# Kernel tuning notes

Measured on AMD Instinct MI355X. Metric: run time of the kernel, lower is better.

Reference implementation:

```python
import jax, jax.numpy as jnp
import numpy as np

B, C, T = 4, 80, 800            # batch, n_mels (= d_model), frames
DEPTH, D_IN, N, DT_R, K = 12, 160, 16, 5, 4  # layers, expand*d_model, d_state, dt_rank, conv kernel
ATT, EMB, EPS = 128, 192, 1e-12

LP_NAMES = ['ln1_g','ln1_b','in_proj','conv_w','conv_b','x_proj','dt_w','dt_b','A_log','D','out_proj','ln2_g','ln2_b','ff_w1','ff_b1','ff_w2','ff_b2']
PP_NAMES = ['att_w1','att_b1','bn1_g','bn1_b','bn1_m','bn1_v','att_w2','att_b2','bn2_g','bn2_b','bn2_m','bn2_v','fc_w','fc_b']


def _layernorm(x, g, b, eps=1e-5):
    mu = x.mean(-1, keepdims=True)
    v = ((x - mu) ** 2).mean(-1, keepdims=True)
    return (x - mu) * jax.lax.rsqrt(v + eps) * g + b


def _mamba(x, p):
    # x: [B, L, d_model] -> standard Mamba selective-scan block
    xz = x @ p['in_proj']                              # [B,L,2*D_IN]
    xc, z = jnp.split(xz, 2, axis=-1)
    xp = jnp.pad(xc, ((0, 0), (K - 1, 0), (0, 0)))     # causal left pad
    xc = jax.lax.conv_general_dilated(
        xp, p['conv_w'], (1,), 'VALID',
        dimension_numbers=('NWC', 'WIO', 'NWC'),
        feature_group_count=D_IN) + p['conv_b']
    xc = jax.nn.silu(xc)
    dbc = xc @ p['x_proj']                             # [B,L,DT_R+2N]
    dt, Bm, Cm = jnp.split(dbc, [DT_R, DT_R + N], axis=-1)
    dt = jax.nn.softplus(dt @ p['dt_w'] + p['dt_b'])   # [B,L,D_IN]
    A = -jnp.exp(p['A_log'])                           # [D_IN,N]

    def step(h, inp):
        x_t, dt_t, B_t, C_t = inp                      # [B,D],[B,D],[B,N],[B,N]
        dA = jnp.exp(dt_t[..., None] * A)              # [B,D,N]
        h = dA * h + (dt_t * x_t)[..., None] * B_t[:, None, :]
        y = jnp.einsum('bdn,bn->bd', h, C_t)
        return h, y

    h0 = jnp.zeros((x.shape[0], D_IN, N), x.dtype)
    xs = tuple(jnp.swapaxes(a, 0, 1) for a in (xc, dt, Bm, Cm))
    _, ys = jax.lax.scan(step, h0, xs)
    y = jnp.swapaxes(ys, 0, 1) + xc * p['D']
    y = y * jax.nn.silu(z)
    return y @ p['out_proj']


def _encoder(x, p):
    xn = _layernorm(x, p['ln1_g'], p['ln1_b'])
    fwd = _mamba(xn, p)
    bwd = jnp.flip(_mamba(jnp.flip(xn, 1), p), 1)      # bidirectional, shared weights
    m = _layernorm(fwd + bwd, p['ln2_g'], p['ln2_b'])
    ff = jax.nn.gelu(m @ p['ff_w1'] + p['ff_b1'], approximate=False) @ p['ff_w2'] + p['ff_b2']
    return ff + x


def _forward(feat, lp, pp):
    feat = feat - feat.mean(-1, keepdims=True)         # CMN
    x = jnp.swapaxes(feat, 1, 2)                       # [B,T,C]

    def body(xc, p):
        return _encoder(xc, p), None

    x, _ = jax.lax.scan(body, x, lp)                   # 12 stacked layers
    x = jnp.swapaxes(x, 1, 2)                          # [B,C,T]

    # Attentive statistics pooling (global context)
    mean = x.mean(-1, keepdims=True)
    std = jnp.sqrt(jnp.maximum(((x - mean) ** 2).mean(-1, keepdims=True), EPS))
    g = jnp.concatenate([x, jnp.broadcast_to(mean, x.shape), jnp.broadcast_to(std, x.shape)], axis=1)  # [B,3C,T]
    a = jnp.einsum('bct,cd->bdt', g, pp['att_w1']) + pp['att_b1'][:, None]
    a = jax.nn.relu(a)
    a = (a - pp['bn1_m'][:, None]) * jax.lax.rsqrt(pp['bn1_v'][:, None] + 1e-5) * pp['bn1_g'][:, None] + pp['bn1_b'][:, None]
    a = jnp.tanh(a)
    a = jnp.einsum('bdt,dc->bct', a, pp['att_w2']) + pp['att_b2'][:, None]
    w = jax.nn.softmax(a, axis=-1)
    mu = jnp.sum(w * x, axis=-1)
    sg = jnp.sqrt(jnp.maximum(jnp.sum(w * x * x, axis=-1) - mu ** 2, EPS))
    pooled = jnp.concatenate([mu, sg], axis=-1)        # [B,2C]

    pooled = (pooled - pp['bn2_m']) * jax.lax.rsqrt(pp['bn2_v'] + 1e-5) * pp['bn2_g'] + pp['bn2_b']
    return pooled @ pp['fc_w'] + pp['fc_b']            # [B,EMB] source embedding


def setup_inputs() -> dict:
    key = jax.random.key(0)
    ks = jax.random.split(key, 12)

    def w(k, shape, s=0.05):
        return jax.random.normal(k, shape, jnp.float32) * s

    L = DEPTH
    return {
        'feat': jax.random.normal(ks[0], (B, C, T), jnp.float32),
        'ln1_g': jnp.ones((L, C)), 'ln1_b': jnp.zeros((L, C)),
        'in_proj': w(ks[1], (L, C, 2 * D_IN)),
        'conv_w': w(ks[2], (L, K, 1, D_IN), 0.2),
        'conv_b': jnp.zeros((L, D_IN)),
        'x_proj': w(ks[3], (L, D_IN, DT_R + 2 * N)),
        'dt_w': w(ks[4], (L, DT_R, D_IN), 0.2),
        'dt_b': jnp.full((L, D_IN), -2.0),
        'A_log': jnp.tile(jnp.log(jnp.arange(1, N + 1, dtype=jnp.float32)), (L, D_IN, 1)),
        'D': jnp.ones((L, D_IN)),
        'out_proj': w(ks[5], (L, D_IN, C)),
        'ln2_g': jnp.ones((L, C)), 'ln2_b': jnp.zeros((L, C)),
        'ff_w1': w(ks[6], (L, C, 4 * C)), 'ff_b1': jnp.zeros((L, 4 * C)),
        'ff_w2': w(ks[7], (L, 4 * C, C)), 'ff_b2': jnp.zeros((L, C)),
        'att_w1': w(ks[8], (3 * C, ATT)), 'att_b1': jnp.zeros((ATT,)),
        'bn1_g': jnp.ones((ATT,)), 'bn1_b': jnp.zeros((ATT,)),
        'bn1_m': jnp.zeros((ATT,)), 'bn1_v': jnp.ones((ATT,)),
        'att_w2': w(ks[9], (ATT, C)), 'att_b2': jnp.zeros((C,)),
        'bn2_g': jnp.ones((2 * C,)), 'bn2_b': jnp.zeros((2 * C,)),
        'bn2_m': jnp.zeros((2 * C,)), 'bn2_v': jnp.ones((2 * C,)),
        'fc_w': w(ks[10], (2 * C, EMB)), 'fc_b': jnp.zeros((EMB,)),
        'aug': 0,
    }


def reference(feat, ln1_g, ln1_b, in_proj, conv_w, conv_b, x_proj, dt_w, dt_b, A_log, D, out_proj, ln2_g, ln2_b, ff_w1, ff_b1, ff_w2, ff_b2, att_w1, att_b1, bn1_g, bn1_b, bn1_m, bn1_v, att_w2, att_b2, bn2_g, bn2_b, bn2_m, bn2_v, fc_w, fc_b, aug):
    lp = dict(zip(LP_NAMES, (ln1_g, ln1_b, in_proj, conv_w, conv_b, x_proj, dt_w, dt_b, A_log, D, out_proj, ln2_g, ln2_b, ff_w1, ff_b1, ff_w2, ff_b2)))
    pp = dict(zip(PP_NAMES, (att_w1, att_b1, bn1_g, bn1_b, bn1_m, bn1_v, att_w2, att_b2, bn2_g, bn2_b, bn2_m, bn2_v, fc_w, fc_b)))
    # aug == 0 -> SpecAug skipped (eval path); speaker branch (frozen, no_grad) omitted
    return _forward(feat, lp, pp)
```

## Files before the change

kernel.cpp:

```cpp
#include <hip/hip_runtime.h>
#include <hip/hip_bf16.h>

#define B_ 4
#define C_ 80
#define T_ 800
#define R_ 3200
#define DIN 160
#define NST 16
#define NC 16
#define LCH 50

typedef const float* fp;

__device__ __forceinline__ void g2l16(const float* g, float* l) {
  __builtin_amdgcn_global_load_lds(
      (const __attribute__((address_space(1))) void*)g,
      (__attribute__((address_space(3))) void*)l,
      16, 0, 0);
}

__device__ __forceinline__ float blockSum(float v, float* sb) {
  for (int o = 32; o; o >>= 1) v += __shfl_xor(v, o);
  __syncthreads();
  if ((threadIdx.x & 63) == 0) sb[threadIdx.x >> 6] = v;
  __syncthreads();
  return sb[0] + sb[1] + sb[2] + sb[3];
}
__device__ __forceinline__ float blockMax(float v, float* sb) {
  for (int o = 32; o; o >>= 1) v = fmaxf(v, __shfl_xor(v, o));
  __syncthreads();
  if ((threadIdx.x & 63) == 0) sb[threadIdx.x >> 6] = v;
  __syncthreads();
  return fmaxf(fmaxf(sb[0], sb[1]), fmaxf(sb[2], sb[3]));
}

__global__ __launch_bounds__(256) void prepw_k(fp in_proj, fp ff_w1,
    fp ln1_g, fp ln1_b, fp ln2_g, fp ln2_b, fp ff_b1,
    float* __restrict__ wp, float* __restrict__ uvb) {
  int idx = blockIdx.x * 256 + threadIdx.x;
  int c = idx % 320, lm = idx / 320;
  int mat = lm & 1, l = lm >> 1;
  fp W = (mat ? ff_w1 : in_proj) + l * 25600;
  fp g = (mat ? ln2_g : ln1_g) + l * 80;
  fp b = (mat ? ln2_b : ln1_b) + l * 80;
  float* wpo = wp + lm * 25600;
  float u = 0.f, v = 0.f;
  for (int k = 0; k < 80; ++k) {
    float w = W[k * 320 + c];
    float gw = g[k] * w;
    wpo[k * 320 + c] = gw;
    u += gw;
    v += b[k] * w;
  }
  if (mat) v += ff_b1[l * 320 + c];
  uvb[lm * 640 + c] = u;
  uvb[lm * 640 + 320 + c] = v;
}

__global__ __launch_bounds__(256) void prepx_k(fp x_proj, float* __restrict__ xpt) {
  int idx = blockIdx.x * 256 + threadIdx.x;
  if (idx >= 71040) return;
  int l = idx / 5920, r = idx % 5920;
  int c = r / 160, k = r % 160;
  xpt[idx] = x_proj[l * 5920 + k * 37 + c];
}

__global__ __launch_bounds__(256) void prept_k(fp out_proj, fp ff_w2,
    float* __restrict__ wot, float* __restrict__ w2t) {
  int idx = blockIdx.x * 256 + threadIdx.x;
  if (idx < 153600) {
    int l = idx / 12800, r = idx % 12800;
    int c = r / 160, k = r % 160;
    wot[idx] = out_proj[l * 12800 + k * 80 + c];
  } else if (idx < 153600 + 307200) {
    int j = idx - 153600;
    int l = j / 25600, r = j % 25600;
    int c = r / 320, k = r % 320;
    w2t[j] = ff_w2[l * 25600 + k * 80 + c];
  }
}

__global__ __launch_bounds__(256) void cmn_k(fp feat, float* __restrict__ x) {
  int bc = blockIdx.x;
  int b = bc / C_, c = bc % C_;
  const float* f = feat + (b * C_ + c) * T_;
  __shared__ float sb[4];
  int tid = threadIdx.x;
  float v[4]; float s = 0.f;
  #pragma unroll
  for (int i = 0; i < 4; ++i) {
    int t = tid + i * 256;
    v[i] = (t < T_) ? f[t] : 0.f;
    s += v[i];
  }
  s = blockSum(s, sb);
  float mu = s * (1.f / T_);
  #pragma unroll
  for (int i = 0; i < 4; ++i) {
    int t = tid + i * 256;
    if (t < T_) x[(b * T_ + t) * C_ + c] = v[i] - mu;
  }
}

__global__ __launch_bounds__(256) void rstat_k(const float* __restrict__ in,
                                               float* __restrict__ must) {
  int row = blockIdx.x * 16 + (threadIdx.x >> 4);
  int c16 = threadIdx.x & 15;
  float s = 0.f, q = 0.f;
  #pragma unroll
  for (int m = 0; m < 5; ++m) {
    float v = in[row * 80 + c16 + 16 * m];
    s += v; q += v * v;
  }
  s += __shfl_xor(s, 1); s += __shfl_xor(s, 2);
  s += __shfl_xor(s, 4); s += __shfl_xor(s, 8);
  q += __shfl_xor(q, 1); q += __shfl_xor(q, 2);
  q += __shfl_xor(q, 4); q += __shfl_xor(q, 8);
  if (c16 == 0) {
    float mu = s * 0.0125f;
    float rs = rsqrtf(fmaxf(q * 0.0125f - mu * mu, 0.f) + 1e-5f);
    must[row * 2] = mu;
    must[row * 2 + 1] = rs;
  }
}

template<int EPI>
__global__ __launch_bounds__(256, 4) void gw_k(const float* __restrict__ A,
    fp W, fp uv, const float* __restrict__ must, const float* __restrict__ extra,
    float* __restrict__ out, int N) {
  __shared__ float SL[5120 + 4 * 1280];
  int tid = threadIdx.x, wv = tid >> 6, ln = tid & 63;
  int bid = blockIdx.x;
// ... 16 lines not shown
  __syncthreads();
  int rq = ln >> 4, c16 = ln & 15;
  float acc[4][4] = {};
  #pragma unroll 2
  for (int k4 = 0; k4 < 80; k4 += 4) {
    float4 a[4], w[4];
    #pragma unroll
    for (int i = 0; i < 4; ++i)
      a[i] = *(const float4*)&As[(rq * 4 + i) * 80 + k4];
    #pragma unroll
    for (int kk = 0; kk < 4; ++kk)
      w[kk] = *(const float4*)&SL[(k4 + kk) * 64 + c16 * 4];
    #pragma unroll
    for (int i = 0; i < 4; ++i) {
      acc[i][0] += a[i].x*w[0].x + a[i].y*w[1].x + a[i].z*w[2].x + a[i].w*w[3].x;
      acc[i][1] += a[i].x*w[0].y + a[i].y*w[1].y + a[i].z*w[2].y + a[i].w*w[3].y;
      acc[i][2] += a[i].x*w[0].z + a[i].y*w[1].z + a[i].z*w[2].z + a[i].w*w[3].z;
      acc[i][3] += a[i].x*w[0].w + a[i].y*w[1].w + a[i].z*w[2].w + a[i].w*w[3].w;
    }
  }
  float ua[4], va[4];
  if (EPI != 3) {
    *(float4*)ua = *(const float4*)&uv[c0 + c16 * 4];
    *(float4*)va = *(const float4*)&uv[N + c0 + c16 * 4];
  }
  #pragma unroll
  for (int i = 0; i < 4; ++i) {
    int row = row0 + rq * 4 + i;
    float mu = 0.f, rs = 1.f;
    if (EPI != 3) {
      float2 ms = *(const float2*)&must[row * 2];
      mu = ms.x; rs = ms.y;
    }
    float4 o;
    float* op = &o.x;
    #pragma unroll
    for (int j = 0; j < 4; ++j) {
      float v = acc[i][j];
      if (EPI == 3) {
        int c = c0 + c16 * 4 + j;
        v += extra[(row / T_) * 128 + c];
        v = fmaxf(v, 0.f);
        v = v * extra[512 + c] + extra[640 + c];
        v = tanhf(v);
      } else {
        v = rs * v - mu * rs * ua[j] + va[j];
      }
      op[j] = v;
    }
    *(float4*)&out[row * N + c0 + c16 * 4] = o;
  }
}

template<int EPI, int KCH, int NKC, int SUM2, int STAT>
__global__ __launch_bounds__(256, 4) void gc_k(const float* __restrict__ A,
    fp W, fp bias, const float* __restrict__ extra, float* __restrict__ out,
    int Astride, float* __restrict__ must) {
  constexpr int P = KCH + 4;
  __shared__ float As[16 * P];
  __shared__ float Wt[80 * P];
  int tid = threadIdx.x;
  int row0 = blockIdx.x * 16;
  int rr = tid >> 4, c16 = tid & 15;
  float acc[5] = {};
  for (int kc = 0; kc < NKC; ++kc) {
    if (kc) __syncthreads();
    #pragma unroll
    for (int i = 0; i < 16 * KCH / 256; ++i) {
      int e = tid + i * 256;
      int r = e / KCH, k = e - r * KCH;
      float v;
      if (SUM2) v = A[(row0 + r) * 320 + k] + A[(row0 + r) * 320 + 160 + k];
      else      v = A[(row0 + r) * Astride + kc * KCH + k];
      As[r * P + k] = v;
    }
    #pragma unroll
    for (int i = 0; i < KCH * 80 / 256; ++i) {
      int e = tid + i * 256;
      int kr = e / 80, c = e - kr * 80;
      Wt[c * P + kr] = W[(kc * KCH + kr) * 80 + c];
    }
    __syncthreads();
    #pragma unroll 4
    for (int k4 = 0; k4 < KCH; k4 += 4) {
      float4 a = *(const float4*)&As[rr * P + k4];
      #pragma unroll
      for (int m = 0; m < 5; ++m) {
        float4 w = *(const float4*)&Wt[(c16 + 16 * m) * P + k4];
        acc[m] += a.x * w.x + a.y * w.y + a.z * w.z + a.w * w.w;
      }
    }
  }
  int row = row0 + rr;
  #pragma unroll
  for (int m = 0; m < 5; ++m) {
    int c = c16 + 16 * m;
    float v = acc[m];
    if (EPI == 2) v += bias[c] + extra[row * 80 + c];
    else if (EPI == 4) v += bias[c];
    out[row * 80 + c] = v;
  }
}

__global__ __launch_bounds__(256, 2) void gof_k(const float* __restrict__ yg,
    fp wotl, fp w1pl, fp uv1, float* __restrict__ g1) {
  __shared__ float As[16 * 164];
  __shared__ float Wt[80 * 164];
  __shared__ float sl[16 * 84];
  __shared__ float ss[32];
  int tid = threadIdx.x, row0 = blockIdx.x * 16, rr = tid >> 4, c16 = tid & 15;
  #pragma unroll
  for (int i = 0; i < 10; ++i) {
    int e = tid + i * 256; int r = e / 160, k = e - r * 160;
    As[r * 164 + k] = yg[(row0 + r) * 320 + k] + yg[(row0 + r) * 320 + 160 + k];
  }
  #pragma unroll
  for (int i = 0; i < 50; ++i) {
    int e = tid + i * 256; int c = e / 160, k = e - c * 160;
    Wt[c * 164 + k] = wotl[e];
  }
  __syncthreads();
  float acc[5] = {};
  #pragma unroll 4
  for (int k4 = 0; k4 < 160; k4 += 4) {
    float4 a = *(const float4*)&As[rr * 164 + k4];
    #pragma unroll
    for (int m = 0; m < 5; ++m) {
      float4 w = *(const float4*)&Wt[(c16 + 16 * m) * 164 + k4];
      acc[m] += a.x * w.x + a.y * w.y + a.z * w.z + a.w * w.w;
    }
  }
  float s = 0.f, q = 0.f;
  #pragma unroll
  for (int m = 0; m < 5; ++m) {
    float v = acc[m];
    sl[rr * 84 + c16 + 16 * m] = v;
    s += v; q += v * v;
  }
  s += __shfl_xor(s, 1); s += __shfl_xor(s, 2);
  s += __shfl_xor(s, 4); s += __shfl_xor(s, 8);
  q += __shfl_xor(q, 1); q += __shfl_xor(q, 2);
  q += __shfl_xor(q, 4); q += __shfl_xor(q, 8);
  if (c16 == 0) {
    float mu = s * 0.0125f;
    ss[rr * 2] = mu;
    ss[rr * 2 + 1] = rsqrtf(fmaxf(q * 0.0125f - mu * mu, 0.f) + 1e-5f);
  }
  for (int h = 0; h < 2; ++h) {
    __syncthreads();
    #pragma unroll
    for (int i = 0; i < 50; ++i) {
      int e = tid + i * 256; int kr = e / 160, c = e - kr * 160;
      Wt[kr * 164 + c] = w1pl[kr * 320 + h * 160 + c];
    }
    __syncthreads();
    float mu = ss[rr * 2], rs = ss[rr * 2 + 1];
    float a2[10] = {};
    for (int k = 0; k < 80; k += 4) {
      float4 av = *(const float4*)&sl[rr * 84 + k];
      #pragma unroll
      for (int m = 0; m < 10; ++m) {
        int c = c16 + 16 * m;
        a2[m] += av.x * Wt[k * 164 + c] + av.y * Wt[(k + 1) * 164 + c]
               + av.z * Wt[(k + 2) * 164 + c] + av.w * Wt[(k + 3) * 164 + c];
      }
    }
    #pragma unroll
    for (int m = 0; m < 10; ++m) {
      int c = h * 160 + c16 + 16 * m;
      float v = rs * a2[m] - mu * rs * uv1[c] + uv1[320 + c];
      v = 0.5f * v * (1.f + erff(v * 0.70710678118f));
      g1[(row0 + rr) * 320 + c] = v;
    }
  }
}

template<int LAST>
__global__ __launch_bounds__(256, 2) void gfi_k(const float* __restrict__ g1,
    fp w2tl, fp fb2, float* __restrict__ x, fp wpn, fp uvn,
    float* __restrict__ xz) {
  __shared__ float As[16 * 164];
  __shared__ float Wt[80 * 164];
  __shared__ float xn[16 * 84];
  __shared__ float ss[32];
  int tid = threadIdx.x, row0 = blockIdx.x * 16, rr = tid >> 4, c16 = tid & 15;
  float acc[5] = {};
  for (int kc = 0; kc < 2; ++kc) {
    if (kc) __syncthreads();
    #pragma unroll
    for (int i = 0; i < 10; ++i) {
      int e = tid + i * 256; int r = e / 160, k = e - r * 160;
      As[r * 164 + k] = g1[(row0 + r) * 320 + kc * 160 + k];
    }
    #pragma unroll
    for (int i = 0; i < 50; ++i) {
      int e = tid + i * 256; int c = e / 160, k = e - c * 160;
      Wt[c * 164 + k] = w2tl[c * 320 + kc * 160 + k];
    }
    __syncthreads();
    #pragma unroll 4
    for (int k4 = 0; k4 < 160; k4 += 4) {
      float4 a = *(const float4*)&As[rr * 164 + k4];
      #pragma unroll
      for (int m = 0; m < 5; ++m) {
        float4 w = *(const float4*)&Wt[(c16 + 16 * m) * 164 + k4];
        acc[m] += a.x * w.x + a.y * w.y + a.z * w.z + a.w * w.w;
      }
    }
  }
  float s = 0.f, q = 0.f;
  #pragma unroll
  for (int m = 0; m < 5; ++m) {
    int c = c16 + 16 * m;
    float v = acc[m] + fb2[c] + x[(row0 + rr) * 80 + c];
    x[(row0 + rr) * 80 + c] = v;
    xn[rr * 84 + c] = v;
    s += v; q += v * v;
  }
  if (!LAST) {
    s += __shfl_xor(s, 1); s += __shfl_xor(s, 2);
    s += __shfl_xor(s, 4); s += __shfl_xor(s, 8);
    q += __shfl_xor(q, 1); q += __shfl_xor(q, 2);
    q += __shfl_xor(q, 4); q += __shfl_xor(q, 8);
    if (c16 == 0) {
      float mu = s * 0.0125f;
      ss[rr * 2] = mu;
      ss[rr * 2 + 1] = rsqrtf(fmaxf(q * 0.0125f - mu * mu, 0.f) + 1e-5f);
    }
    for (int h = 0; h < 2; ++h) {
      __syncthreads();
      #pragma unroll
      for (int i = 0; i < 50; ++i) {
        int e = tid + i * 256; int kr = e / 160, c = e - kr * 160;
        Wt[kr * 164 + c] = wpn[kr * 320 + h * 160 + c];
      }
      __syncthreads();
      float mu = ss[rr * 2], rs = ss[rr * 2 + 1];
      float a2[10] = {};
      for (int k = 0; k < 80; k += 4) {
        float4 av = *(const float4*)&xn[rr * 84 + k];
        #pragma unroll
        for (int m = 0; m < 10; ++m) {
          int c = c16 + 16 * m;
          a2[m] += av.x * Wt[k * 164 + c] + av.y * Wt[(k + 1) * 164 + c]
                 + av.z * Wt[(k + 2) * 164 + c] + av.w * Wt[(k + 3) * 164 + c];
        }
      }
      #pragma unroll
      for (int m = 0; m < 10; ++m) {
        int c = h * 160 + c16 + 16 * m;
        xz[(row0 + rr) * 320 + c] = rs * a2[m] - mu * rs * uvn[c] + uvn[320 + c];
      }
    }
  }
}

__global__ __launch_bounds__(256) void cxf_k(const float* __restrict__ xz,
    fp cw, fp cb, fp xptl, fp dtw, fp dtb,
    float* __restrict__ xcf, float* __restrict__ xcbb,
    float* __restrict__ dbc2, float* __restrict__ dt2) {
  __shared__ float As[16 * 164];
  __shared__ float xpT[37 * 164];
  __shared__ float dbcl[16 * 40];
  int bi = blockIdx.x;
  int tc = bi % 50; int rem = bi / 50;
  int b = rem & 3, dir = rem >> 2;
  int t0 = tc * 16;
  int tid = threadIdx.x;
  #pragma unroll
  for (int i = 0; i < 24; ++i) {
    int e = tid + i * 256;
    if (e < 5920) {
      int c = e / 160, k = e - c * 160;
      xpT[c * 164 + k] = xptl[e];
    }
  }
  float* xco = dir ? xcbb : xcf;
  #pragma unroll
  for (int i = 0; i < 3; ++i) {
    int e = tid + i * 256;
    if (e < 640) {
      int ii = e / 40, d4 = (e - ii * 40) * 4;
      int t = t0 + ii;
      float4 acc = *(const float4*)&cb[d4];
      #pragma unroll
      for (int k = 0; k < 4; ++k) {
        int tt = t - 3 + k;
        if (tt >= 0) {
          int src = dir ? (T_ - 1 - tt) : tt;
          float4 xv = *(const float4*)&xz[(b * T_ + src) * 320 + d4];
          float4 wv = *(const float4*)&cw[k * DIN + d4];
          acc.x += wv.x * xv.x; acc.y += wv.y * xv.y;
          acc.z += wv.z * xv.z; acc.w += wv.w * xv.w;
        }
      }
      float4 o;
      o.x = acc.x / (1.f + __expf(-acc.x));
      o.y = acc.y / (1.f + __expf(-acc.y));
      o.z = acc.z / (1.f + __expf(-acc.z));
      o.w = acc.w / (1.f + __expf(-acc.w));
      *(float4*)&As[ii * 164 + d4] = o;
      *(float4*)&xco[(b * T_ + t) * DIN + d4] = o;
    }
  }
  __syncthreads();
  int rr = tid >> 4, c16 = tid & 15;
  int grow0 = dir * R_ + b * T_ + t0;
  {
    float a0 = 0.f, a1 = 0.f, a2 = 0.f;
    for (int k4 = 0; k4 < 160; k4 += 4) {
      float4 a = *(const float4*)&As[rr * 164 + k4];
      float4 w0 = *(const float4*)&xpT[c16 * 164 + k4];
      float4 w1 = *(const float4*)&xpT[(c16 + 16) * 164 + k4];
      a0 += a.x * w0.x + a.y * w0.y + a.z * w0.z + a.w * w0.w;
      a1 += a.x * w1.x + a.y * w1.y + a.z * w1.z + a.w * w1.w;
      if (c16 < 5) {
        float4 w2 = *(const float4*)&xpT[(c16 + 32) * 164 + k4];
        a2 += a.x * w2.x + a.y * w2.y + a.z * w2.z + a.w * w2.w;
      }
    }
    dbcl[rr * 40 + c16] = a0;
    dbcl[rr * 40 + c16 + 16] = a1;
    dbc2[(grow0 + rr) * 37 + c16] = a0;
    dbc2[(grow0 + rr) * 37 + c16 + 16] = a1;
    if (c16 < 5) {
      dbcl[rr * 40 + c16 + 32] = a2;
      dbc2[(grow0 + rr) * 37 + c16 + 32] = a2;
    }
  }
  __syncthreads();
  #pragma unroll
  for (int i = 0; i < 10; ++i) {
    int e = tid + i * 256;
    int ii = e / 160, d = e - ii * 160;
    float v = dtb[d];
    #pragma unroll
    for (int m = 0; m < 5; ++m) v += dbcl[ii * 40 + m] * dtw[m * DIN + d];
    v = fmaxf(v, 0.f) + __logf(1.f + __expf(-fabsf(v)));
    dt2[(grow0 + ii) * DIN + d] = v;
  }
}

__global__ __launch_bounds__(256) void scanA_k(const float* __restrict__ dt2,
    const float* __restrict__ xcf, const float* __restrict__ xcbb,
    const float* __restrict__ dbc2, fp A_log,
    float* __restrict__ hend, float* __restrict__ pprod) {
  int bi = blockIdx.x;
  int cch = bi % NC; int rem = bi / NC;
  int dblk = rem % 10; rem /= 10;
  int b = rem % 4; int dir = rem / 4;
  int d0 = dblk * 16;
  int tid = threadIdx.x, dl = tid >> 4, n = tid & 15;
  int d = d0 + dl;
  float Areg = -__expf(A_log[d * NST + n]);
  __shared__ float sdt[LCH][16], sdx[LCH][16], sB[LCH][16];
  const float* xc = dir ? xcbb : xcf;
  int rbase = dir * R_ + b * T_ + cch * LCH;
  int rloc0 = b * T_ + cch * LCH;
  for (int e = tid; e < LCH * 16; e += 256) {
    int i = e >> 4, jj = e & 15;
    int grow = rbase + i;
    float dtv = dt2[grow * DIN + d0 + jj];
    sdt[i][jj] = dtv;
    sdx[i][jj] = dtv * xc[(rloc0 + i) * DIN + d0 + jj];
    sB[i][jj]  = dbc2[grow * 37 + 5 + jj];
  }
  __syncthreads();
  float h = 0.f, dts = 0.f;
  #pragma unroll 2
  for (int i = 0; i < LCH; ++i) {
    float dtv = sdt[i][dl];
    float a = __expf(dtv * Areg);
    h = a * h + sdx[i][dl] * sB[i][n];
    dts += dtv;
  }
  hend[bi * 256 + tid] = h;
  pprod[bi * 256 + tid] = __expf(dts * Areg);
}

__global__ __launch_bounds__(256) void scanC_k(const float* __restrict__ dt2,
    const float* __restrict__ dbc2, const float* __restrict__ xcf,
    const float* __restrict__ xcbb, const float* __restrict__ xz,
    fp A_log, fp Dp, const float* __restrict__ hend,
    const float* __restrict__ pprod, float* __restrict__ ygcat) {
  int bi = blockIdx.x;
  int cch = bi % NC; int rem = bi / NC;
  int dblk = rem % 10; rem /= 10;
  int b = rem % 4; int dir = rem / 4;
  int d0 = dblk * 16;
  int tid = threadIdx.x, dl = tid >> 4, n = tid & 15;
  int d = d0 + dl;
  float Areg = -__expf(A_log[d * NST + n]);
  __shared__ float sdt[LCH][16], sdx[LCH][16], sB[LCH][16], sC[LCH][16];
  __shared__ float sY[LCH][16];
  const float* xc = dir ? xcbb : xcf;
  int rbase = dir * R_ + b * T_ + cch * LCH;
  int rloc0 = b * T_ + cch * LCH;
  int sbase = (bi / NC) * (NC * 256) + tid;
  float h = 0.f;
  #pragma unroll
  for (int cc = 0; cc < NC; ++cc) {
    float p = pprod[sbase + cc * 256];
    float e = hend[sbase + cc * 256];
    if (cc < cch) h = p * h + e;
  }
  for (int e = tid; e < LCH * 16; e += 256) {
    int i = e >> 4, jj = e & 15;
    int grow = rbase + i;
    float dtv = dt2[grow * DIN + d0 + jj];
    sdt[i][jj] = dtv;
    sdx[i][jj] = dtv * xc[(rloc0 + i) * DIN + d0 + jj];
    sB[i][jj]  = dbc2[grow * 37 + 5 + jj];
    sC[i][jj]  = dbc2[grow * 37 + 21 + jj];
  }
  __syncthreads();
  for (int i = 0; i < LCH; ++i) {
    float a = __expf(sdt[i][dl] * Areg);
    h = a * h + sdx[i][dl] * sB[i][n];
    float y = h * sC[i][n];
    y += __shfl_xor(y, 1);
    y += __shfl_xor(y, 2);
    y += __shfl_xor(y, 4);
    y += __shfl_xor(y, 8);
    if (n == 0) sY[i][dl] = y;
  }
  __syncthreads();
  for (int e = tid; e < LCH * 16; e += 256) {
    int i = e >> 4, jj = e & 15;
    int t = cch * LCH + i;
    int rloc = b * T_ + t;
    float xcv = xc[rloc * DIN + d0 + jj];
    int orow = dir ? (b * T_ + (T_ - 1 - t)) : rloc;
    float z = xz[orow * 320 + 160 + d0 + jj];
    float sg = 1.f / (1.f + __expf(-z));
    ygcat[orow * 320 + dir * 160 + d0 + jj] = (sY[i][jj] + xcv * Dp[d0 + jj]) * (z * sg);
  }
}

__global__ __launch_bounds__(256) void stats_k(const float* __restrict__ x,
                                               float* __restrict__ meanv, float* __restrict__ stdv) {
  int bc = blockIdx.x; int b = bc / C_, c = bc % C_;
  __shared__ float sb[4];
  int tid = threadIdx.x;
  float v[4]; float s = 0.f;
  #pragma unroll
  for (int i = 0; i < 4; ++i) {
    int t = tid + i * 256;
    v[i] = (t < T_) ? x[(b * T_ + t) * C_ + c] : 0.f;
    s += v[i];
  }
  s = blockSum(s, sb);
  float mu = s * (1.f / T_);
  float q = 0.f;
  #pragma unroll
  for (int i = 0; i < 4; ++i) {
    int t = tid + i * 256;
    if (t < T_) { float dd = v[i] - mu; q += dd * dd; }
  }
  q = blockSum(q, sb);
  if (tid == 0) { meanv[bc] = mu; stdv[bc] = sqrtf(fmaxf(q * (1.f / T_), 1e-12f)); }
}

__global__ __launch_bounds__(256) void prep_k(const float* __restrict__ meanv,
    const float* __restrict__ stdv, fp w1, fp ab1, fp g1p, fp b1p, fp m1p, fp v1p,
    float* __restrict__ pack) {
  int idx = blockIdx.x * 256 + threadIdx.x;
  if (idx < 512) {
    int b = idx / 128, dcol = idx % 128;
    float acc = ab1[dcol];
    for (int c = 0; c < C_; ++c) {
      acc += meanv[b * C_ + c] * w1[(C_ + c) * 128 + dcol];
      acc += stdv[b * C_ + c] * w1[(2 * C_ + c) * 128 + dcol];
    }
    pack[idx] = acc;
  } else if (idx < 640) {
    int dcol = idx - 512;
    float kv = g1p[dcol] * rsqrtf(v1p[dcol] + 1e-5f);
    pack[512 + dcol] = kv;
    pack[640 + dcol] = b1p[dcol] - m1p[dcol] * kv;
  }
}

__global__ __launch_bounds__(256) void pool_k(const float* __restrict__ x,
    const float* __restrict__ scores, fp g2, fp b2, fp m2, fp v2,
    float* __restrict__ pooledn) {
  int bc = blockIdx.x; int b = bc / C_, c = bc % C_;
  __shared__ float sb[4];
  int tid = threadIdx.x;
// ... 24 lines not shown
    pooledn[b * 160 + j1] = (sg - m2[j1]) * rsqrtf(v2[j1] + 1e-5f) * g2[j1] + b2[j1];
  }
}

__global__ __launch_bounds__(256) void fc_k(const float* __restrict__ pooledn, fp fw, fp fb,
                                            float* __restrict__ out) {
  int idx = blockIdx.x * 256 + threadIdx.x;
  if (idx >= 4 * 192) return;
  int b = idx / 192, e = idx % 192;
  float acc = fb[e];
  for (int i = 0; i < 160; ++i) acc += pooledn[b * 160 + i] * fw[i * 192 + e];
  out[idx] = acc;
}

extern "C" void kernel_launch(void* const* d_in, const int* in_sizes, int n_in,
                              void* d_out, int out_size, void* d_ws, size_t ws_size,
                              hipStream_t stream) {
  fp feat   = (fp)d_in[0];
  fp ln1_g  = (fp)d_in[1];  fp ln1_b  = (fp)d_in[2];
  fp in_proj= (fp)d_in[3];
  fp conv_w = (fp)d_in[4];  fp conv_b = (fp)d_in[5];
  fp x_proj = (fp)d_in[6];
  fp dt_w   = (fp)d_in[7];  fp dt_b   = (fp)d_in[8];
  fp A_log  = (fp)d_in[9];  fp Dp     = (fp)d_in[10];
  fp out_proj=(fp)d_in[11];
  fp ln2_g  = (fp)d_in[12]; fp ln2_b  = (fp)d_in[13];
  fp ff_w1  = (fp)d_in[14]; fp ff_b1  = (fp)d_in[15];
  fp ff_w2  = (fp)d_in[16]; fp ff_b2  = (fp)d_in[17];
  fp att_w1 = (fp)d_in[18]; fp att_b1 = (fp)d_in[19];
  fp bn1_g  = (fp)d_in[20]; fp bn1_b  = (fp)d_in[21];
  fp bn1_m  = (fp)d_in[22]; fp bn1_v  = (fp)d_in[23];
  fp att_w2 = (fp)d_in[24]; fp att_b2 = (fp)d_in[25];
  fp bn2_g  = (fp)d_in[26]; fp bn2_b  = (fp)d_in[27];
  fp bn2_m  = (fp)d_in[28]; fp bn2_v  = (fp)d_in[29];
  fp fc_w   = (fp)d_in[30]; fp fc_b   = (fp)d_in[31];

  float* ws   = (float*)d_ws;
  float* x    = ws;
  float* xz   = ws + 256000;
  float* xcf  = ws + 1280000;
  float* xcb  = ws + 1792000;
  float* dbc2 = ws + 2304000;
  float* dt2  = ws + 2540800;
  float* hend = ws + 3564800;
  float* pprod= ws + 3892480;
  float* ygcat= ws + 4220160;
  float* meanv= ws + 5244160;
  float* stdv = ws + 5244480;
  float* pack = ws + 5244800;
  float* pooledn = ws + 5245568;
  float* wp   = ws + 5246208;
  float* uvb  = ws + 5860608;
  float* mst_x= ws + 5875968;
  float* xpt  = ws + 5882368;
  float* wot  = ws + 5953408;
  float* w2t  = ws + 6107008;
  float* g1   = xz;
  float* a1b  = hend;
  float* sc   = dt2;

  prepw_k<<<30, 256, 0, stream>>>(in_proj, ff_w1, ln1_g, ln1_b, ln2_g, ln2_b,
                                  ff_b1, wp, uvb);
  prepx_k<<<278, 256, 0, stream>>>(x_proj, xpt);
  prept_k<<<1800, 256, 0, stream>>>(out_proj, ff_w2, wot, w2t);
  cmn_k<<<320, 256, 0, stream>>>(feat, x);
  rstat_k<<<200, 256, 0, stream>>>(x, mst_x);
  gw_k<0><<<250, 256, 0, stream>>>(x, wp, uvb, mst_x, nullptr, xz, 320);

  for (int l = 0; l < 12; ++l) {
    cxf_k<<<400, 256, 0, stream>>>(xz, conv_w + l * 640, conv_b + l * 160,
                                   xpt + l * 5920, dt_w + l * 800, dt_b + l * 160,
                                   xcf, xcb, dbc2, dt2);
    scanA_k<<<1280, 256, 0, stream>>>(dt2, xcf, xcb, dbc2, A_log + l * 2560, hend, pprod);
    scanC_k<<<1280, 256, 0, stream>>>(dt2, dbc2, xcf, xcb, xz, A_log + l * 2560,
                                      Dp + l * 160, hend, pprod, ygcat);
    gof_k<<<200, 256, 0, stream>>>(ygcat, wot + l * 12800, wp + (2 * l + 1) * 25600,
                                   uvb + (2 * l + 1) * 640, g1);
    if (l < 11)
      gfi_k<0><<<200, 256, 0, stream>>>(g1, w2t + l * 25600, ff_b2 + l * 80, x,
                                        wp + (2 * l + 2) * 25600,
                                        uvb + (2 * l + 2) * 640, xz);
    else
      gfi_k<1><<<200, 256, 0, stream>>>(g1, w2t + l * 25600, ff_b2 + l * 80, x,
                                        wp, uvb, xz);
  }

  stats_k<<<320, 256, 0, stream>>>(x, meanv, stdv);
  prep_k<<<3, 256, 0, stream>>>(meanv, stdv, att_w1, att_b1, bn1_g, bn1_b, bn1_m, bn1_v, pack);
  gw_k<3><<<100, 256, 0, stream>>>(x, att_w1, nullptr, nullptr, pack, a1b, 128);
  gc_k<4, 128, 1, 0, 0><<<200, 256, 0, stream>>>(a1b, att_w2, att_b2, nullptr, sc, 128, nullptr);
  pool_k<<<320, 256, 0, stream>>>(x, sc, bn2_g, bn2_b, bn2_m, bn2_v, pooledn);
  fc_k<<<3, 256, 0, stream>>>(pooledn, fc_w, fc_b, (float*)d_out);
}
```

Baseline: 1.262 ms.

## Pre-pad weight tiles and stage them via direct global-to-LDS loads

A prep kernel now writes every per-layer weight matrix (out_proj, ff_w1 halves, ff_w2 halves, next-layer in_proj halves, x_proj) into the exact padded shared-memory layout, with stride 164. The GEMM kernels can then copy them straight into LDS with 16-byte global_load_lds instead of per-element transposing loads. The scan kernels likewise stage dt, x, B and C with 4-byte global_load_lds, and the scanC epilogue reuses the staged x instead of reloading it. The aim is to cut VGPR round trips and address math during staging. The cost is extra prep work and a larger workspace for the padded weight copies.

```diff
diff --git a/kernel.cpp b/kernel.cpp
--- a/kernel.cpp
+++ b/kernel.cpp
@@ -17,6 +17,26 @@
       (const __attribute__((address_space(1))) void*)g,
       (__attribute__((address_space(3))) void*)l,
       16, 0, 0);
+}
+__device__ __forceinline__ void g2l4(const float* g, float* l) {
+  __builtin_amdgcn_global_load_lds(
+      (const __attribute__((address_space(1))) void*)g,
+      (__attribute__((address_space(3))) void*)l,
+      4, 0, 0);
+}
+
+template<int NF4>
+__device__ __forceinline__ void stageN(float* dst, const float* src, int tid) {
+  int wv = tid >> 6, ln = tid & 63;
+  constexpr int NP = (NF4 + 255) / 256;
+  #pragma unroll
+  for (int i = 0; i < NP; ++i) {
+    int cbase = i * 256 + wv * 64;
+    if (cbase + ln < NF4) {
+      int lo = __builtin_amdgcn_readfirstlane(cbase * 4);
+      g2l16(src + (cbase + ln) * 4, dst + lo);
+    }
+  }
 }
 
 __device__ __forceinline__ float blockSum(float v, float* sb) {
@@ -57,27 +77,38 @@
   uvb[lm * 640 + 320 + c] = v;
 }
 
-__global__ __launch_bounds__(256) void prepx_k(fp x_proj, float* __restrict__ xpt) {
+__global__ __launch_bounds__(256) void prepg_k(fp out_proj, fp ff_w2,
+    const float* __restrict__ wp, float* __restrict__ wotp,
+    float* __restrict__ w1pp, float* __restrict__ w2tp, float* __restrict__ wpnp) {
   int idx = blockIdx.x * 256 + threadIdx.x;
-  if (idx >= 71040) return;
-  int l = idx / 5920, r = idx % 5920;
-  int c = r / 160, k = r % 160;
-  xpt[idx] = x_proj[l * 5920 + k * 37 + c];
-}
-
-__global__ __launch_bounds__(256) void prept_k(fp out_proj, fp ff_w2,
-    float* __restrict__ wot, float* __restrict__ w2t) {
+  if (idx >= 1102080) return;
+  int l = idx / 91840, r = idx % 91840;
+  if (r < 13120) {
+    int c = r / 164, k = r % 164;
+    wotp[l * 13120 + r] = (k < 160) ? out_proj[l * 12800 + k * 80 + c] : 0.f;
+  } else if (r < 39360) {
+    int r2 = r - 13120; int h = r2 / 13120, r3 = r2 % 13120;
+    int kr = r3 / 164, cq = r3 % 164;
+    w1pp[l * 26240 + r2] = (cq < 160) ? wp[(2 * l + 1) * 25600 + kr * 320 + h * 160 + cq] : 0.f;
+  } else if (r < 65600) {
+    int r2 = r - 39360; int h = r2 / 13120, r3 = r2 % 13120;
+    int c = r3 / 164, k = r3 % 164;
+    w2tp[l * 26240 + r2] = (k < 160) ? ff_w2[l * 25600 + (h * 160 + k) * 80 + c] : 0.f;
+  } else {
+    int r2 = r - 65600; int h = r2 / 13120, r3 = r2 % 13120;
+    int kr = r3 / 164, cq = r3 % 164;
+    float v = 0.f;
+    if (l < 11 && cq < 160) v = wp[(2 * l + 2) * 25600 + kr * 320 + h * 160 + cq];
+    wpnp[l * 26240 + r2] = v;
+  }
+}
+
+__global__ __launch_bounds__(256) void prepx_k(fp x_proj, float* __restrict__ xptp) {
   int idx = blockIdx.x * 256 + threadIdx.x;
-  if (idx < 153600) {
-    int l = idx / 12800, r = idx % 12800;
-    int c = r / 160, k = r % 160;
-    wot[idx] = out_proj[l * 12800 + k * 80 + c];
-  } else if (idx < 153600 + 307200) {
-    int j = idx - 153600;
-    int l = j / 25600, r = j % 25600;
-    int c = r / 320, k = r % 320;
-    w2t[j] = ff_w2[l * 25600 + k * 80 + c];
-  }
+  if (idx >= 72816) return;
+  int l = idx / 6068, r = idx % 6068;
+  int c = r / 164, k = r % 164;
+  xptp[idx] = (k < 160) ? x_proj[l * 5920 + k * 37 + c] : 0.f;
 }
 
 __global__ __launch_bounds__(256) void cmn_k(fp feat, float* __restrict__ x) {
@@ -200,10 +231,9 @@
   }
 }
 
-template<int EPI, int KCH, int NKC, int SUM2, int STAT>
+template<int EPI, int KCH, int NKC>
 __global__ __launch_bounds__(256, 4) void gc_k(const float* __restrict__ A,
-    fp W, fp bias, const float* __restrict__ extra, float* __restrict__ out,
-    int Astride, float* __restrict__ must) {
+    fp W, fp bias, float* __restrict__ out, int Astride) {
   constexpr int P = KCH + 4;
   __shared__ float As[16 * P];
   __shared__ float Wt[80 * P];
@@ -217,10 +247,7 @@
     for (int i = 0; i < 16 * KCH / 256; ++i) {
       int e = tid + i * 256;
       int r = e / KCH, k = e - r * KCH;
-      float v;
-      if (SUM2) v = A[(row0 + r) * 320 + k] + A[(row0 + r) * 320 + 160 + k];
-      else      v = A[(row0 + r) * Astride + kc * KCH + k];
-      As[r * P + k] = v;
+      As[r * P + k] = A[(row0 + r) * Astride + kc * KCH + k];
     }
     #pragma unroll
     for (int i = 0; i < KCH * 80 / 256; ++i) {
@@ -244,162 +271,8 @@
   for (int m = 0; m < 5; ++m) {
     int c = c16 + 16 * m;
     float v = acc[m];
-    if (EPI == 2) v += bias[c] + extra[row * 80 + c];
-    else if (EPI == 4) v += bias[c];
+    if (EPI == 4) v += bias[c];
     out[row * 80 + c] = v;
-  }
-}
-
-__global__ __launch_bounds__(256, 2) void gof_k(const float* __restrict__ yg,
-    fp wotl, fp w1pl, fp uv1, float* __restrict__ g1) {
-  __shared__ float As[16 * 164];
-  __shared__ float Wt[80 * 164];
-  __shared__ float sl[16 * 84];
-  __shared__ float ss[32];
-  int tid = threadIdx.x, row0 = blockIdx.x * 16, rr = tid >> 4, c16 = tid & 15;
-  #pragma unroll
-  for (int i = 0; i < 10; ++i) {
-    int e = tid + i * 256; int r = e / 160, k = e - r * 160;
-    As[r * 164 + k] = yg[(row0 + r) * 320 + k] + yg[(row0 + r) * 320 + 160 + k];
-  }
-  #pragma unroll
-  for (int i = 0; i < 50; ++i) {
-    int e = tid + i * 256; int c = e / 160, k = e - c * 160;
-    Wt[c * 164 + k] = wotl[e];
-  }
-  __syncthreads();
-  float acc[5] = {};
-  #pragma unroll 4
-  for (int k4 = 0; k4 < 160; k4 += 4) {
-    float4 a = *(const float4*)&As[rr * 164 + k4];
-    #pragma unroll
-    for (int m = 0; m < 5; ++m) {
-      float4 w = *(const float4*)&Wt[(c16 + 16 * m) * 164 + k4];
-      acc[m] += a.x * w.x + a.y * w.y + a.z * w.z + a.w * w.w;
-    }
-  }
-  float s = 0.f, q = 0.f;
-  #pragma unroll
-  for (int m = 0; m < 5; ++m) {
-    float v = acc[m];
-    sl[rr * 84 + c16 + 16 * m] = v;
-    s += v; q += v * v;
-  }
-  s += __shfl_xor(s, 1); s += __shfl_xor(s, 2);
-  s += __shfl_xor(s, 4); s += __shfl_xor(s, 8);
-  q += __shfl_xor(q, 1); q += __shfl_xor(q, 2);
-  q += __shfl_xor(q, 4); q += __shfl_xor(q, 8);
-  if (c16 == 0) {
-    float mu = s * 0.0125f;
-    ss[rr * 2] = mu;
-    ss[rr * 2 + 1] = rsqrtf(fmaxf(q * 0.0125f - mu * mu, 0.f) + 1e-5f);
-  }
-  for (int h = 0; h < 2; ++h) {
-    __syncthreads();
-    #pragma unroll
-    for (int i = 0; i < 50; ++i) {
-      int e = tid + i * 256; int kr = e / 160, c = e - kr * 160;
-      Wt[kr * 164 + c] = w1pl[kr * 320 + h * 160 + c];
-    }
-    __syncthreads();
-    float mu = ss[rr * 2], rs = ss[rr * 2 + 1];
-    float a2[10] = {};
-    for (int k = 0; k < 80; k += 4) {
-      float4 av = *(const float4*)&sl[rr * 84 + k];
-      #pragma unroll
-      for (int m = 0; m < 10; ++m) {
-        int c = c16 + 16 * m;
-        a2[m] += av.x * Wt[k * 164 + c] + av.y * Wt[(k + 1) * 164 + c]
-               + av.z * Wt[(k + 2) * 164 + c] + av.w * Wt[(k + 3) * 164 + c];
-      }
-    }
-    #pragma unroll
-    for (int m = 0; m < 10; ++m) {
-      int c = h * 160 + c16 + 16 * m;
-      float v = rs * a2[m] - mu * rs * uv1[c] + uv1[320 + c];
-      v = 0.5f * v * (1.f + erff(v * 0.70710678118f));
-      g1[(row0 + rr) * 320 + c] = v;
-    }
-  }
-}
-
-template<int LAST>
-__global__ __launch_bounds__(256, 2) void gfi_k(const float* __restrict__ g1,
-    fp w2tl, fp fb2, float* __restrict__ x, fp wpn, fp uvn,
-    float* __restrict__ xz) {
-  __shared__ float As[16 * 164];
-  __shared__ float Wt[80 * 164];
-  __shared__ float xn[16 * 84];
-  __shared__ float ss[32];
-  int tid = threadIdx.x, row0 = blockIdx.x * 16, rr = tid >> 4, c16 = tid & 15;
-  float acc[5] = {};
-  for (int kc = 0; kc < 2; ++kc) {
-    if (kc) __syncthreads();
-    #pragma unroll
-    for (int i = 0; i < 10; ++i) {
-      int e = tid + i * 256; int r = e / 160, k = e - r * 160;
-      As[r * 164 + k] = g1[(row0 + r) * 320 + kc * 160 + k];
-    }
-    #pragma unroll
-    for (int i = 0; i < 50; ++i) {
-      int e = tid + i * 256; int c = e / 160, k = e - c * 160;
-      Wt[c * 164 + k] = w2tl[c * 320 + kc * 160 + k];
-    }
-    __syncthreads();
-    #pragma unroll 4
-    for (int k4 = 0; k4 < 160; k4 += 4) {
-      float4 a = *(const float4*)&As[rr * 164 + k4];
-      #pragma unroll
-      for (int m = 0; m < 5; ++m) {
-        float4 w = *(const float4*)&Wt[(c16 + 16 * m) * 164 + k4];
-        acc[m] += a.x * w.x + a.y * w.y + a.z * w.z + a.w * w.w;
-      }
-    }
-  }
-  float s = 0.f, q = 0.f;
-  #pragma unroll
-  for (int m = 0; m < 5; ++m) {
-    int c = c16 + 16 * m;
-    float v = acc[m] + fb2[c] + x[(row0 + rr) * 80 + c];
-    x[(row0 + rr) * 80 + c] = v;
-    xn[rr * 84 + c] = v;
-    s += v; q += v * v;
-  }
-  if (!LAST) {
-    s += __shfl_xor(s, 1); s += __shfl_xor(s, 2);
-    s += __shfl_xor(s, 4); s += __shfl_xor(s, 8);
-    q += __shfl_xor(q, 1); q += __shfl_xor(q, 2);
-    q += __shfl_xor(q, 4); q += __shfl_xor(q, 8);
-    if (c16 == 0) {
-      float mu = s * 0.0125f;
-      ss[rr * 2] = mu;
-      ss[rr * 2 + 1] = rsqrtf(fmaxf(q * 0.0125f - mu * mu, 0.f) + 1e-5f);
-    }
-    for (int h = 0; h < 2; ++h) {
-      __syncthreads();
-      #pragma unroll
-      for (int i = 0; i < 50; ++i) {
-        int e = tid + i * 256; int kr = e / 160, c = e - kr * 160;
-        Wt[kr * 164 + c] = wpn[kr * 320 + h * 160 + c];
-      }
-      __syncthreads();
-      float mu = ss[rr * 2], rs = ss[rr * 2 + 1];
-      float a2[10] = {};
-      for (int k = 0; k < 80; k += 4) {
-        float4 av = *(const float4*)&xn[rr * 84 + k];
-        #pragma unroll
-        for (int m = 0; m < 10; ++m) {
-          int c = c16 + 16 * m;
-          a2[m] += av.x * Wt[k * 164 + c] + av.y * Wt[(k + 1) * 164 + c]
-                 + av.z * Wt[(k + 2) * 164 + c] + av.w * Wt[(k + 3) * 164 + c];
-        }
-      }
-      #pragma unroll
-      for (int m = 0; m < 10; ++m) {
-        int c = h * 160 + c16 + 16 * m;
-        xz[(row0 + rr) * 320 + c] = rs * a2[m] - mu * rs * uvn[c] + uvn[320 + c];
-      }
-    }
   }
 }
 
@@ -415,14 +288,7 @@
   int b = rem & 3, dir = rem >> 2;
   int t0 = tc * 16;
   int tid = threadIdx.x;
-  #pragma unroll
-  for (int i = 0; i < 24; ++i) {
-    int e = tid + i * 256;
-    if (e < 5920) {
-      int c = e / 160, k = e - c * 160;
-      xpT[c * 164 + k] = xptl[e];
-    }
-  }
+  stageN<1517>(xpT, xptl, tid);
   float* xco = dir ? xcbb : xcf;
   #pragma unroll
   for (int i = 0; i < 3; ++i) {
@@ -493,6 +359,7 @@
     const float* __restrict__ xcf, const float* __restrict__ xcbb,
     const float* __restrict__ dbc2, fp A_log,
     float* __restrict__ hend, float* __restrict__ pprod) {
+  __shared__ float sdt[800], sX[800], sB[800];
   int bi = blockIdx.x;
   int cch = bi % NC; int rem = bi / NC;
   int dblk = rem % 10; rem /= 10;
@@ -500,26 +367,30 @@
   int d0 = dblk * 16;
   int tid = threadIdx.x, dl = tid >> 4, n = tid & 15;
   int d = d0 + dl;
-  float Areg = -__expf(A_log[d * NST + n]);
-  __shared__ float sdt[LCH][16], sdx[LCH][16], sB[LCH][16];
   const float* xc = dir ? xcbb : xcf;
   int rbase = dir * R_ + b * T_ + cch * LCH;
   int rloc0 = b * T_ + cch * LCH;
-  for (int e = tid; e < LCH * 16; e += 256) {
-    int i = e >> 4, jj = e & 15;
-    int grow = rbase + i;
-    float dtv = dt2[grow * DIN + d0 + jj];
-    sdt[i][jj] = dtv;
-    sdx[i][jj] = dtv * xc[(rloc0 + i) * DIN + d0 + jj];
-    sB[i][jj]  = dbc2[grow * 37 + 5 + jj];
-  }
+  int wv = tid >> 6, ln = tid & 63;
+  #pragma unroll
+  for (int i = 0; i < 4; ++i) {
+    int cbase = i * 256 + wv * 64;
+    int e = cbase + ln;
+    if (e < 800) {
+      int ii = e >> 4, jj = e & 15;
+      int lo = __builtin_amdgcn_readfirstlane(cbase);
+      g2l4(dt2 + (rbase + ii) * DIN + d0 + jj, sdt + lo);
+      g2l4(xc + (rloc0 + ii) * DIN + d0 + jj, sX + lo);
+      g2l4(dbc2 + (rbase + ii) * 37 + 5 + jj, sB + lo);
+    }
+  }
+  float Areg = -__expf(A_log[d * NST + n]);
   __syncthreads();
   float h = 0.f, dts = 0.f;
   #pragma unroll 2
   for (int i = 0; i < LCH; ++i) {
-    float dtv = sdt[i][dl];
-    float a = __expf(dtv * Areg);
-    h = a * h + sdx[i][dl] * sB[i][n];
+    float dtv = sdt[i * 16 + dl];
+    float aa = __expf(dtv * Areg);
+    h = aa * h + dtv * sX[i * 16 + dl] * sB[i * 16 + n];
     dts += dtv;
   }
   hend[bi * 256 + tid] = h;
@@ -531,6 +402,7 @@
     const float* __restrict__ xcbb, const float* __restrict__ xz,
     fp A_log, fp Dp, const float* __restrict__ hend,
     const float* __restrict__ pprod, float* __restrict__ ygcat) {
+  __shared__ float sdt[800], sX[800], sB[800], sC[800], sY[800];
   int bi = blockIdx.x;
   int cch = bi % NC; int rem = bi / NC;
   int dblk = rem % 10; rem /= 10;
@@ -538,12 +410,24 @@
   int d0 = dblk * 16;
   int tid = threadIdx.x, dl = tid >> 4, n = tid & 15;
   int d = d0 + dl;
-  float Areg = -__expf(A_log[d * NST + n]);
-  __shared__ float sdt[LCH][16], sdx[LCH][16], sB[LCH][16], sC[LCH][16];
-  __shared__ float sY[LCH][16];
   const float* xc = dir ? xcbb : xcf;
   int rbase = dir * R_ + b * T_ + cch * LCH;
   int rloc0 = b * T_ + cch * LCH;
+  int wv = tid >> 6, ln = tid & 63;
+  #pragma unroll
+  for (int i = 0; i < 4; ++i) {
+    int cbase = i * 256 + wv * 64;
+    int e = cbase + ln;
+    if (e < 800) {
+      int ii = e >> 4, jj = e & 15;
+      int lo = __builtin_amdgcn_readfirstlane(cbase);
+      g2l4(dt2 + (rbase + ii) * DIN + d0 + jj, sdt + lo);
+      g2l4(xc + (rloc0 + ii) * DIN + d0 + jj, sX + lo);
+      g2l4(dbc2 + (rbase + ii) * 37 + 5 + jj, sB + lo);
+      g2l4(dbc2 + (rbase + ii) * 37 + 21 + jj, sC + lo);
+    }
+  }
+  float Areg = -__expf(A_log[d * NST + n]);
   int sbase = (bi / NC) * (NC * 256) + tid;
   float h = 0.f;
   #pragma unroll
@@ -552,36 +436,172 @@
     float e = hend[sbase + cc * 256];
     if (cc < cch) h = p * h + e;
   }
-  for (int e = tid; e < LCH * 16; e += 256) {
-    int i = e >> 4, jj = e & 15;
-    int grow = rbase + i;
-    float dtv = dt2[grow * DIN + d0 + jj];
-    sdt[i][jj] = dtv;
-    sdx[i][jj] = dtv * xc[(rloc0 + i) * DIN + d0 + jj];
-    sB[i][jj]  = dbc2[grow * 37 + 5 + jj];
-    sC[i][jj]  = dbc2[grow * 37 + 21 + jj];
-  }
   __syncthreads();
   for (int i = 0; i < LCH; ++i) {
-    float a = __expf(sdt[i][dl] * Areg);
-    h = a * h + sdx[i][dl] * sB[i][n];
-    float y = h * sC[i][n];
+    float dtv = sdt[i * 16 + dl];
+    float a = __expf(dtv * Areg);
+    h = a * h + dtv * sX[i * 16 + dl] * sB[i * 16 + n];
+    float y = h * sC[i * 16 + n];
     y += __shfl_xor(y, 1);
     y += __shfl_xor(y, 2);
     y += __shfl_xor(y, 4);
     y += __shfl_xor(y, 8);
-    if (n == 0) sY[i][dl] = y;
+    if (n == 0) sY[i * 16 + dl] = y;
   }
   __syncthreads();
   for (int e = tid; e < LCH * 16; e += 256) {
     int i = e >> 4, jj = e & 15;
     int t = cch * LCH + i;
-    int rloc = b * T_ + t;
-    float xcv = xc[rloc * DIN + d0 + jj];
-    int orow = dir ? (b * T_ + (T_ - 1 - t)) : rloc;
+    float xcv = sX[i * 16 + jj];
+    int orow = dir ? (b * T_ + (T_ - 1 - t)) : (b * T_ + t);
     float z = xz[orow * 320 + 160 + d0 + jj];
     float sg = 1.f / (1.f + __expf(-z));
-    ygcat[orow * 320 + dir * 160 + d0 + jj] = (sY[i][jj] + xcv * Dp[d0 + jj]) * (z * sg);
+    ygcat[orow * 320 + dir * 160 + d0 + jj] = (sY[i * 16 + jj] + xcv * Dp[d0 + jj]) * (z * sg);
+  }
+}
+
+__global__ __launch_bounds__(256, 2) void gof_k(const float* __restrict__ yg,
+    fp wotp_l, fp w1pp_l, fp uv1, float* __restrict__ g1) {
+  __shared__ float S[17120];
+  float* Wt = S;
+  float* As = S + 13120;
+  float* sl = S + 15744;
+  float* ss = S + 17088;
+  int tid = threadIdx.x, row0 = blockIdx.x * 16, rr = tid >> 4, c16 = tid & 15;
+  stageN<3280>(Wt, wotp_l, tid);
+  #pragma unroll
+  for (int i = 0; i < 10; ++i) {
+    int e = tid + i * 256; int r = e / 160, k = e - r * 160;
+    As[r * 164 + k] = yg[(row0 + r) * 320 + k] + yg[(row0 + r) * 320 + 160 + k];
+  }
+  __syncthreads();
+  {
+    float acc[5] = {};
+    #pragma unroll 4
+    for (int k4 = 0; k4 < 160; k4 += 4) {
+      float4 a = *(const float4*)&As[rr * 164 + k4];
+      #pragma unroll
+      for (int m = 0; m < 5; ++m) {
+        float4 w = *(const float4*)&Wt[(c16 + 16 * m) * 164 + k4];
+        acc[m] += a.x * w.x + a.y * w.y + a.z * w.z + a.w * w.w;
+      }
+    }
+    float s = 0.f, q = 0.f;
+    #pragma unroll
+    for (int m = 0; m < 5; ++m) {
+      float v = acc[m];
+      sl[rr * 84 + c16 + 16 * m] = v;
+      s += v; q += v * v;
+    }
+    s += __shfl_xor(s, 1); s += __shfl_xor(s, 2);
+    s += __shfl_xor(s, 4); s += __shfl_xor(s, 8);
+    q += __shfl_xor(q, 1); q += __shfl_xor(q, 2);
+    q += __shfl_xor(q, 4); q += __shfl_xor(q, 8);
+    if (c16 == 0) {
+      float mu = s * 0.0125f;
+      ss[rr * 2] = mu;
+      ss[rr * 2 + 1] = rsqrtf(fmaxf(q * 0.0125f - mu * mu, 0.f) + 1e-5f);
+    }
+  }
+  for (int h = 0; h < 2; ++h) {
+    __syncthreads();
+    stageN<3280>(Wt, w1pp_l + h * 13120, tid);
+    __syncthreads();
+    float mu = ss[rr * 2], rs = ss[rr * 2 + 1];
+    float a2[10] = {};
+    for (int k = 0; k < 80; k += 4) {
+      float4 av = *(const float4*)&sl[rr * 84 + k];
+      #pragma unroll
+      for (int m = 0; m < 10; ++m) {
+        int c = c16 + 16 * m;
+        a2[m] += av.x * Wt[k * 164 + c] + av.y * Wt[(k + 1) * 164 + c]
+               + av.z * Wt[(k + 2) * 164 + c] + av.w * Wt[(k + 3) * 164 + c];
+      }
+    }
+    #pragma unroll
+    for (int m = 0; m < 10; ++m) {
+      int c = h * 160 + c16 + 16 * m;
+      float v = rs * a2[m] - mu * rs * uv1[c] + uv1[320 + c];
+      v = 0.5f * v * (1.f + erff(v * 0.70710678118f));
+      g1[(row0 + rr) * 320 + c] = v;
+    }
+  }
+}
+
+template<int LAST>
+__global__ __launch_bounds__(256, 2) void gfi_k(const float* __restrict__ g1,
+    fp w2tp_l, fp fb2, float* __restrict__ x, fp wpnp_l, fp uvn,
+    float* __restrict__ xz) {
+  __shared__ float S[17120];
+  float* Wt = S;
+  float* As = S + 13120;
+  float* xn = S + 15744;
+  float* ss = S + 17088;
+  int tid = threadIdx.x, row0 = blockIdx.x * 16, rr = tid >> 4, c16 = tid & 15;
+  float acc2[5] = {};
+  for (int kc = 0; kc < 2; ++kc) {
+    if (kc) __syncthreads();
+    stageN<3280>(Wt, w2tp_l + kc * 13120, tid);
+    #pragma unroll
+    for (int i = 0; i < 10; ++i) {
+      int e = tid + i * 256; int r = e / 160, k = e - r * 160;
+      As[r * 164 + k] = g1[(row0 + r) * 320 + kc * 160 + k];
+    }
+    __syncthreads();
+    #pragma unroll 4
+    for (int k4 = 0; k4 < 160; k4 += 4) {
+      float4 a = *(const float4*)&As[rr * 164 + k4];
+      #pragma unroll
+      for (int m = 0; m < 5; ++m) {
+        float4 w = *(const float4*)&Wt[(c16 + 16 * m) * 164 + k4];
+        acc2[m] += a.x * w.x + a.y * w.y + a.z * w.z + a.w * w.w;
+      }
+    }
+  }
+  {
+    float s = 0.f, q = 0.f;
+    #pragma unroll
+    for (int m = 0; m < 5; ++m) {
+      int c = c16 + 16 * m;
+      float v = acc2[m] + fb2[c] + x[(row0 + rr) * 80 + c];
+      x[(row0 + rr) * 80 + c] = v;
+      xn[rr * 84 + c] = v;
+      s += v; q += v * v;
+    }
+    if (!LAST) {
+      s += __shfl_xor(s, 1); s += __shfl_xor(s, 2);
+      s += __shfl_xor(s, 4); s += __shfl_xor(s, 8);
+      q += __shfl_xor(q, 1); q += __shfl_xor(q, 2);
+      q += __shfl_xor(q, 4); q += __shfl_xor(q, 8);
+      if (c16 == 0) {
+        float mu = s * 0.0125f;
+        ss[rr * 2] = mu;
+        ss[rr * 2 + 1] = rsqrtf(fmaxf(q * 0.0125f - mu * mu, 0.f) + 1e-5f);
+      }
+    }
+  }
+  if (!LAST) {
+    for (int h = 0; h < 2; ++h) {
+      __syncthreads();
+      stageN<3280>(Wt, wpnp_l + h * 13120, tid);
+      __syncthreads();
+      float mu = ss[rr * 2], rs = ss[rr * 2 + 1];
+      float a3[10] = {};
+      for (int k = 0; k < 80; k += 4) {
+        float4 av = *(const float4*)&xn[rr * 84 + k];
+        #pragma unroll
+        for (int m = 0; m < 10; ++m) {
+          int c = c16 + 16 * m;
+          a3[m] += av.x * Wt[k * 164 + c] + av.y * Wt[(k + 1) * 164 + c]
+                 + av.z * Wt[(k + 2) * 164 + c] + av.w * Wt[(k + 3) * 164 + c];
+        }
+      }
+      #pragma unroll
+      for (int m = 0; m < 10; ++m) {
+        int c = h * 160 + c16 + 16 * m;
+        xz[(row0 + rr) * 320 + c] = rs * a3[m] - mu * rs * uvn[c] + uvn[320 + c];
+      }
+    }
   }
 }
 
@@ -712,43 +732,45 @@
   float* wp   = ws + 5246208;
   float* uvb  = ws + 5860608;
   float* mst_x= ws + 5875968;
-  float* xpt  = ws + 5882368;
-  float* wot  = ws + 5953408;
-  float* w2t  = ws + 6107008;
+  float* xptp = ws + 5882368;
+  float* wotp = ws + 5955184;
+  float* w1pp = ws + 6112624;
+  float* w2tp = ws + 6427504;
+  float* wpnp = ws + 6742384;
   float* g1   = xz;
   float* a1b  = hend;
   float* sc   = dt2;
 
   prepw_k<<<30, 256, 0, stream>>>(in_proj, ff_w1, ln1_g, ln1_b, ln2_g, ln2_b,
                                   ff_b1, wp, uvb);
-  prepx_k<<<278, 256, 0, stream>>>(x_proj, xpt);
-  prept_k<<<1800, 256, 0, stream>>>(out_proj, ff_w2, wot, w2t);
+  prepg_k<<<4305, 256, 0, stream>>>(out_proj, ff_w2, wp, wotp, w1pp, w2tp, wpnp);
+  prepx_k<<<285, 256, 0, stream>>>(x_proj, xptp);
   cmn_k<<<320, 256, 0, stream>>>(feat, x);
   rstat_k<<<200, 256, 0, stream>>>(x, mst_x);
   gw_k<0><<<250, 256, 0, stream>>>(x, wp, uvb, mst_x, nullptr, xz, 320);
 
   for (int l = 0; l < 12; ++l) {
     cxf_k<<<400, 256, 0, stream>>>(xz, conv_w + l * 640, conv_b + l * 160,
-                                   xpt + l * 5920, dt_w + l * 800, dt_b + l * 160,
+                                   xptp + l * 6068, dt_w + l * 800, dt_b + l * 160,
                                    xcf, xcb, dbc2, dt2);
-    scanA_k<<<1280, 256, 0, stream>>>(dt2, xcf, xcb, dbc2, A_log + l * 2560, hend, pprod);
+    scanA_k<<<1280, 256, 0, stream>>>(dt2, xcf, xcb, dbc2, A_log + l * 2560,
+                                      hend, pprod);
     scanC_k<<<1280, 256, 0, stream>>>(dt2, dbc2, xcf, xcb, xz, A_log + l * 2560,
                                       Dp + l * 160, hend, pprod, ygcat);
-    gof_k<<<200, 256, 0, stream>>>(ygcat, wot + l * 12800, wp + (2 * l + 1) * 25600,
+    gof_k<<<200, 256, 0, stream>>>(ygcat, wotp + l * 13120, w1pp + l * 26240,
                                    uvb + (2 * l + 1) * 640, g1);
     if (l < 11)
-      gfi_k<0><<<200, 256, 0, stream>>>(g1, w2t + l * 25600, ff_b2 + l * 80, x,
-                                        wp + (2 * l + 2) * 25600,
-                                        uvb + (2 * l + 2) * 640, xz);
+      gfi_k<0><<<200, 256, 0, stream>>>(g1, w2tp + l * 26240, ff_b2 + l * 80, x,
+                                        wpnp + l * 26240, uvb + (2 * l + 2) * 640, xz);
     else
-      gfi_k<1><<<200, 256, 0, stream>>>(g1, w2t + l * 25600, ff_b2 + l * 80, x,
-                                        wp, uvb, xz);
+      gfi_k<1><<<200, 256, 0, stream>>>(g1, w2tp + l * 26240, ff_b2 + l * 80, x,
+                                        wpnp + l * 26240, uvb, xz);
   }
 
   stats_k<<<320, 256, 0, stream>>>(x, meanv, stdv);
   prep_k<<<3, 256, 0, stream>>>(meanv, stdv, att_w1, att_b1, bn1_g, bn1_b, bn1_m, bn1_v, pack);
   gw_k<3><<<100, 256, 0, stream>>>(x, att_w1, nullptr, nullptr, pack, a1b, 128);
-  gc_k<4, 128, 1, 0, 0><<<200, 256, 0, stream>>>(a1b, att_w2, att_b2, nullptr, sc, 128, nullptr);
+  gc_k<4, 128, 1><<<200, 256, 0, stream>>>(a1b, att_w2, att_b2, sc, 128);
   pool_k<<<320, 256, 0, stream>>>(x, sc, bn2_g, bn2_b, bn2_m, bn2_v, pooledn);
   fc_k<<<3, 256, 0, stream>>>(pooledn, fc_w, fc_b, (float*)d_out);
 }
```

Result: faster. 1.172 ms (-7.1%).
